# Performance work log

Hardware: AMD Instinct MI355X
Metric: run time of the kernel (lower is better)

## Reference

```python
import jax, jax.numpy as jnp
import numpy as np

N = 100000   # nodes
E = 1000000  # edges (before self-loops)
D_IN = 16
H, C = 2, 64  # heads, hidden per head
EPS = 1e-5    # BatchNorm eps
SLOPE = 0.2   # LeakyReLU negative slope (GATConv default)


def setup_inputs() -> dict:
    key = jax.random.key(0)
    ks = jax.random.split(key, 40)
    rn = lambda k, s, sc=0.1: jax.random.normal(k, s, jnp.float32) * sc
    inp = {}
    inp["x"] = jax.random.normal(ks[0], (N, D_IN), jnp.float32)
    inp["edge_index"] = jax.random.randint(ks[1], (2, E), 0, N)
    i = 2
    for l, din in ((1, D_IN), (2, C), (3, C)):
        inp[f"W{l}"] = rn(ks[i], (din, H * C)); i += 1
        inp[f"as{l}"] = rn(ks[i], (H, C)); i += 1
        inp[f"ad{l}"] = rn(ks[i], (H, C)); i += 1
        inp[f"b{l}"] = jnp.zeros((C,), jnp.float32)
        inp[f"g{l}"] = jnp.ones((C,), jnp.float32)   # BN gamma
        inp[f"be{l}"] = jnp.zeros((C,), jnp.float32) # BN beta
    inp["mW1"] = rn(ks[i], (C + 5, C)); i += 1
    inp["mb1"] = jnp.zeros((C,), jnp.float32)
    inp["mW2"] = rn(ks[i], (C, C)); i += 1
    inp["mb2"] = jnp.zeros((C,), jnp.float32)
    inp["pW"] = rn(ks[i], (C, 1)); i += 1
    inp["pb"] = jnp.zeros((1,), jnp.float32)
    inp["vW"] = rn(ks[i], (C, 1)); i += 1
    inp["vb"] = jnp.zeros((1,), jnp.float32)
    return inp


def gat(x, src, dst, W, att_s, att_d, bias):
    # GATConv, heads=H, concat=False (mean over heads). Messages flow src->dst.
    h = (x @ W).reshape(-1, H, C)               # [N,H,C]
    a_s = jnp.sum(h * att_s, -1)                # [N,H]
    a_d = jnp.sum(h * att_d, -1)                # [N,H]
    e = jax.nn.leaky_relu(a_s[src] + a_d[dst], SLOPE)  # [Etot,H]
    e = e - jax.ops.segment_max(e, dst, num_segments=N)[dst]
    ee = jnp.exp(e)
    alpha = ee / (jax.ops.segment_sum(ee, dst, num_segments=N)[dst] + 1e-16)
    msg = h[src] * alpha[:, :, None]            # [Etot,H,C]
    out = jax.ops.segment_sum(msg, dst, num_segments=N)  # [N,H,C]
    return out.mean(1) + bias                   # [N,C]


def bn(h, g, b):
    m = h.mean(0)
    v = jnp.mean((h - m) ** 2, 0)  # biased variance (torch BN normalization)
    return (h - m) * jax.lax.rsqrt(v + EPS) * g + b


def reference(x, edge_index, W1, as1, ad1, b1, g1, be1,
              W2, as2, ad2, b2, g2, be2, W3, as3, ad3, b3, g3, be3,
              mW1, mb1, mW2, mb2, pW, pb, vW, vb):
    loops = jnp.arange(N)
    src = jnp.concatenate([edge_index[0], loops])  # add_self_loops=True
    dst = jnp.concatenate([edge_index[1], loops])
    ctx = x[:, 9:14]  # context features [N,5]
    h = jax.nn.relu(bn(gat(x, src, dst, W1, as1, ad1, b1), g1, be1))
    h = jax.nn.relu(bn(gat(h, src, dst, W2, as2, ad2, b2), g2, be2))
    h = jax.nn.relu(bn(gat(h, src, dst, W3, as3, ad3, b3), g3, be3))
    # dropout is identity in eval reference
    h = jnp.concatenate([h, ctx], axis=1)          # [N, C+5]
    h = jax.nn.relu(h @ mW1 + mb1) @ mW2 + mb2     # MLP
    logits = (h @ pW + pb).squeeze(-1)             # [N]
    value = (h @ vW + vb).squeeze(-1)              # [N]
    return logits, value
```

## Files before the change

### kernel.cpp

```cpp
#include <hip/hip_runtime.h>
#include <hip/hip_fp16.h>


__device__ __forceinline__ float leaky(float x) { return x > 0.f ? x : 0.2f * x; }

typedef float f32x4 __attribute__((ext_vector_type(4)));

#define BCAP 4096
#define NSL 256

__global__ void bucket_hist(const int* __restrict__ dst, int* __restrict__ bcnt, int E) {
  __shared__ int cnt[512];
  int t = threadIdx.x;
  cnt[t] = 0; cnt[t + 256] = 0;
  __syncthreads();
  for (int e = blockIdx.x * blockDim.x + t; e < E; e += gridDim.x * blockDim.x)
    atomicAdd(&cnt[dst[e] >> 8], 1);
  __syncthreads();
  for (int i = t; i < 512; i += 256)
    if (cnt[i]) atomicAdd(&bcnt[i], cnt[i]);
}

__global__ void bucket_scan(const int* __restrict__ bcnt, int* __restrict__ boff,
                            int* __restrict__ bcur, int nbk) {
  __shared__ int temp[512];
  int t = threadIdx.x;
  int v = (t < nbk) ? bcnt[t] : 0;
  temp[t] = v;
  __syncthreads();
  for (int off = 1; off < 512; off <<= 1) {
    int add = (t >= off) ? temp[t - off] : 0;
    __syncthreads();
    temp[t] += add;
    __syncthreads();
  }
  if (t < nbk) {
    int ex = temp[t] - v;
    boff[t] = ex;
    bcur[t] = ex;
  }
}

__global__ __launch_bounds__(256) void bin_scatter(
    const int* __restrict__ src, const int* __restrict__ dst,
    int* __restrict__ bcur, int2* __restrict__ ebuf, int E) {
  __shared__ int cnt[512];
  __shared__ int base[512];
  int t = threadIdx.x;
  int beg = blockIdx.x * 8192;
  int end = min(E, beg + 8192);
  cnt[t] = 0; cnt[t + 256] = 0;
  __syncthreads();
  for (int e = beg + t; e < end; e += 256)
    atomicAdd(&cnt[dst[e] >> 8], 1);
  __syncthreads();
  for (int i = t; i < 512; i += 256) {
    base[i] = cnt[i] ? atomicAdd(&bcur[i], cnt[i]) : 0;
    cnt[i] = 0;
  }
  __syncthreads();
  for (int e = beg + t; e < end; e += 256) {
    int d = dst[e];
    int bk = d >> 8;
    int off = atomicAdd(&cnt[bk], 1);
    ebuf[base[bk] + off] = make_int2(src[e], d);
  }
}

__global__ __launch_bounds__(256) void bucket_sort(
    const int2* __restrict__ ebuf, const int* __restrict__ boff,
    int2* __restrict__ col2, int* __restrict__ row_ptr, int E, int n, int nbk) {
  __shared__ int2 eds[BCAP];
  __shared__ int dcnt[256];
  __shared__ int dbase[256];
  __shared__ int dexcl[256];
  int b = blockIdx.x, t = threadIdx.x;
  int S = boff[b];
  int Eend = (b + 1 < nbk) ? boff[b + 1] : E;
  int cnt = min(Eend - S, BCAP);
  for (int i = t; i < cnt; i += 256) eds[i] = ebuf[S + i];
  dcnt[t] = 0;
  __syncthreads();
  for (int i = t; i < cnt; i += 256) atomicAdd(&dcnt[eds[i].y & 255], 1);
  __syncthreads();
  int v = dcnt[t];
  dbase[t] = v;
  __syncthreads();
  for (int off = 1; off < 256; off <<= 1) {
    int add = (t >= off) ? dbase[t - off] : 0;
    __syncthreads();
    dbase[t] += add;
    __syncthreads();
  }
  int excl = dbase[t] - v;
  int d = (b << 8) + t;
  if (d < n) row_ptr[d] = S + excl;
  if (b == nbk - 1 && t == 0) row_ptr[n] = E;
  dcnt[t] = 0;
  dexcl[t] = excl;
  __syncthreads();
  for (int i = t; i < cnt; i += 256) {
    int2 e = eds[i];
    int dl = e.y & 255;
    int off = atomicAdd(&dcnt[dl], 1);
    col2[S + dexcl[dl] + off] = e;
  }
}

__global__ __launch_bounds__(256) void bn_stats(const float* __restrict__ h,
                                                float* __restrict__ stats, int n) {
  __shared__ float ssum[64], ssq[64];
  int t = threadIdx.x;
  if (t < 64) { ssum[t] = 0.f; ssq[t] = 0.f; }
  __syncthreads();
  const float4* h4 = (const float4*)h;
  size_t total4 = (size_t)n * 16;
  size_t stride = (size_t)gridDim.x * blockDim.x;
  int cbase = ((int)(((size_t)blockIdx.x * blockDim.x + t) & 15)) * 4;
  float s0 = 0.f, s1 = 0.f, s2 = 0.f, s3 = 0.f;
  float q0 = 0.f, q1 = 0.f, q2 = 0.f, q3 = 0.f;
  for (size_t i = (size_t)blockIdx.x * blockDim.x + t; i < total4; i += stride) {
    float4 v = h4[i];
    s0 += v.x; q0 = fmaf(v.x, v.x, q0);
    s1 += v.y; q1 = fmaf(v.y, v.y, q1);
    s2 += v.z; q2 = fmaf(v.z, v.z, q2);
    s3 += v.w; q3 = fmaf(v.w, v.w, q3);
  }
  atomicAdd(&ssum[cbase + 0], s0); atomicAdd(&ssq[cbase + 0], q0);
  atomicAdd(&ssum[cbase + 1], s1); atomicAdd(&ssq[cbase + 1], q1);
  atomicAdd(&ssum[cbase + 2], s2); atomicAdd(&ssq[cbase + 2], q2);
  atomicAdd(&ssum[cbase + 3], s3); atomicAdd(&ssq[cbase + 3], q3);
  __syncthreads();
  if (t < 64) {
    stats[blockIdx.x * 128 + t] = ssum[t];
    stats[blockIdx.x * 128 + 64 + t] = ssq[t];
  }
}

__global__ void bn_finalize(const float* __restrict__ stats, const float* __restrict__ g,
                            const float* __restrict__ be, float* __restrict__ scsh,
                            float inv_n) {
  __shared__ float red[128];
  int t = threadIdx.x;
  int c = t & 63;
  int off = (t >> 6) * 64;
  float acc = 0.f;
  for (int b = 0; b < NSL; b++) acc += stats[b * 128 + off + c];
  red[t] = acc;
  __syncthreads();
  if (t < 64) {
    float mean = red[t] * inv_n;
    float var = red[64 + t] * inv_n - mean * mean;
    float sc = rsqrtf(var + 1e-5f) * g[t];
    scsh[t] = sc;
    scsh[64 + t] = be[t] - mean * sc;
  }
}

template <int K, bool BN>
__global__ __launch_bounds__(256) void gat_project_tiled(
    const float* __restrict__ act, const float* __restrict__ scsh,
    const float* __restrict__ W,
    const float* __restrict__ att_s, const float* __restrict__ att_d,
    __half2* __restrict__ hb, float* __restrict__ as_,
    float* __restrict__ ad_, int n) {
  constexpr int AST = K + 4;
  __shared__ float aS[64 * AST];
  __shared__ float wS[K * 128];
  __shared__ float attS[256];

  int t = threadIdx.x;
  int node0 = blockIdx.x * 64;
  int rows = min(64, n - node0);

  constexpr int AF4 = 64 * K / 4;
  for (int i = t; i < AF4; i += 256) {
    int r = i / (K / 4), kc = i % (K / 4);
    float4 v = make_float4(0.f, 0.f, 0.f, 0.f);
    if (r < rows) v = *(const float4*)&act[(size_t)(node0 + r) * K + kc * 4];
    if (BN) {
      float4 sc4 = *(const float4*)&scsh[kc * 4];
      float4 sh4 = *(const float4*)&scsh[64 + kc * 4];
      v.x = fmaxf(fmaf(v.x, sc4.x, sh4.x), 0.f);
      v.y = fmaxf(fmaf(v.y, sc4.y, sh4.y), 0.f);
      v.z = fmaxf(fmaf(v.z, sc4.z, sh4.z), 0.f);
      v.w = fmaxf(fmaf(v.w, sc4.w, sh4.w), 0.f);
    }
    *(float4*)&aS[r * AST + kc * 4] = v;
  }
  constexpr int WF4 = K * 32;
  for (int i = t; i < WF4; i += 256)
    *(float4*)&wS[i * 4] = *(const float4*)&W[i * 4];
  attS[t] = (t < 128) ? att_s[t] : att_d[t - 128];
  __syncthreads();

  int tc = t & 15, tr = t >> 4;
  int c0 = tc * 8, r0 = tr * 4;

  float acc[4][8] = {};
  for (int k = 0; k < K; k += 4) {
    float4 av[4];
    float4 wv[4][2];
#pragma unroll
    for (int i = 0; i < 4; i++) av[i] = *(const float4*)&aS[(r0 + i) * AST + k];
#pragma unroll
    for (int kk = 0; kk < 4; kk++) {
      wv[kk][0] = *(const float4*)&wS[(k + kk) * 128 + c0];
      wv[kk][1] = *(const float4*)&wS[(k + kk) * 128 + c0 + 4];
    }
#pragma unroll
    for (int i = 0; i < 4; i++) {
      const float* ai = (const float*)&av[i];
#pragma unroll
      for (int kk = 0; kk < 4; kk++) {
        const float* w0 = (const float*)&wv[kk][0];
        const float* w1 = (const float*)&wv[kk][1];
#pragma unroll
        for (int j = 0; j < 4; j++) {
          acc[i][j] = fmaf(ai[kk], w0[j], acc[i][j]);
          acc[i][4 + j] = fmaf(ai[kk], w1[j], acc[i][4 + j]);
        }
      }
    }
  }

#pragma unroll
  for (int i = 0; i < 4; i++) {
    int r = r0 + i;
    float psv = 0.f, pdv = 0.f;
#pragma unroll
    for (int j = 0; j < 8; j++) {
      psv = fmaf(acc[i][j], attS[c0 + j], psv);
      pdv = fmaf(acc[i][j], attS[128 + c0 + j], pdv);
    }
    psv += __shfl_xor(psv, 1); pdv += __shfl_xor(pdv, 1);
    psv += __shfl_xor(psv, 2); pdv += __shfl_xor(pdv, 2);
    psv += __shfl_xor(psv, 4); pdv += __shfl_xor(pdv, 4);
    if (r < rows) {
      size_t base = (size_t)(node0 + r) * 64 + (c0 >> 1);
      hb[base + 0] = __floats2half2_rn(acc[i][0], acc[i][1]);
      hb[base + 1] = __floats2half2_rn(acc[i][2], acc[i][3]);
      hb[base + 2] = __floats2half2_rn(acc[i][4], acc[i][5]);
      hb[base + 3] = __floats2half2_rn(acc[i][6], acc[i][7]);
      if (tc == 0 || tc == 8) {
        int head = tc >> 3;
        as_[(node0 + r) * 2 + head] = psv;
        ad_[(node0 + r) * 2 + head] = pdv;
      }
    }
  }
}

__device__ __forceinline__ void fma8(float* a, float my, uint4 raw) {
  float2 f;
  f = __half22float2(__builtin_bit_cast(__half2, raw.x)); a[0] = fmaf(my, f.x, a[0]); a[1] = fmaf(my, f.y, a[1]);
  f = __half22float2(__builtin_bit_cast(__half2, raw.y)); a[2] = fmaf(my, f.x, a[2]); a[3] = fmaf(my, f.y, a[3]);
  f = __half22float2(__builtin_bit_cast(__half2, raw.z)); a[4] = fmaf(my, f.x, a[4]); a[5] = fmaf(my, f.y, a[5]);
  f = __half22float2(__builtin_bit_cast(__half2, raw.w)); a[6] = fmaf(my, f.x, a[6]); a[7] = fmaf(my, f.y, a[7]);
}

__global__ __launch_bounds__(256) void gat_aggregate(
    const __half2* __restrict__ hb,
    const float* __restrict__ as_, const float* __restrict__ ad_,
    const int* __restrict__ row_ptr, const int2* __restrict__ col2,
    const float* __restrict__ bias, float* __restrict__ out, int n) {
  int wave = (int)((blockIdx.x * blockDim.x + threadIdx.x) >> 6);
  int lane = threadIdx.x & 63;
  if (wave >= n) return;
  int d = wave;
  int sub = lane >> 4, q = lane & 15;
  bool head1 = (q >= 8);
  int hidx = head1 ? 1 : 0;
  int beg = row_ptr[d], end = row_ptr[d + 1];
  const uint4* hb4 = (const uint4*)hb;

  float2 dv = *(const float2*)&ad_[d * 2];
  float ad_my = head1 ? dv.y : dv.x;

  float a[8] = {};
  float dpart = 0.f;

  if (sub == 0) {
    float asv = as_[d * 2 + hidx];
    float my = __expf(leaky(asv + ad_my));
    uint4 raw = hb4[(size_t)d * 16 + q];
    fma8(a, my, raw);
    dpart = my;
  }

  int k = beg;
  for (; k + 7 < end; k += 8) {
    int kkA = k + sub, kkB = k + 4 + sub;
    int sA = col2[kkA].x;
    int sB = col2[kkB].x;
    float asA = as_[sA * 2 + hidx];
    float asB = as_[sB * 2 + hidx];
    uint4 rawA = hb4[(size_t)sA * 16 + q];
    uint4 rawB = hb4[(size_t)sB * 16 + q];
    float myA = __expf(leaky(asA + ad_my));
    float myB = __expf(leaky(asB + ad_my));
    fma8(a, myA, rawA);
    dpart += myA;
    fma8(a, myB, rawB);
    dpart += myB;
  }
  if (k + 3 < end) {
    int kk = k + sub;
    int s = col2[kk].x;
    float asv = as_[s * 2 + hidx];
    uint4 raw = hb4[(size_t)s * 16 + q];
    float my = __expf(leaky(asv + ad_my));
    fma8(a, my, raw);
    dpart += my;
    k += 4;
  }
  int rem = end - k;
  if (sub < rem) {
    int kk = k + sub;
    int s = col2[kk].x;
    float asv = as_[s * 2 + hidx];
    uint4 raw = hb4[(size_t)s * 16 + q];
    float my = __expf(leaky(asv + ad_my));
    fma8(a, my, raw);
    dpart += my;
  }

#pragma unroll
  for (int i = 0; i < 8; i++) a[i] += __shfl(a[i], lane ^ 16);
  dpart += __shfl(dpart, lane ^ 16);
#pragma unroll
  for (int i = 0; i < 8; i++) a[i] += __shfl(a[i], lane ^ 32);
  float dsum = dpart + __shfl(dpart, lane ^ 32);

  int src = (lane + 8) & 63;
  float b[8];
#pragma unroll
  for (int i = 0; i < 8; i++) b[i] = __shfl(a[i], src);
  float den1 = __shfl(dsum, src);
  if (lane < 8) {
    float r0 = 1.f / (dsum + 1e-16f), r1 = 1.f / (den1 + 1e-16f);
    float4 bl = *(const float4*)&bias[q * 8];
    float4 bh = *(const float4*)&bias[q * 8 + 4];
    f32x4 o0, o1;
    o0.x = 0.5f * (a[0] * r0 + b[0] * r1) + bl.x;
    o0.y = 0.5f * (a[1] * r0 + b[1] * r1) + bl.y;
    o0.z = 0.5f * (a[2] * r0 + b[2] * r1) + bl.z;
    o0.w = 0.5f * (a[3] * r0 + b[3] * r1) + bl.w;
    o1.x = 0.5f * (a[4] * r0 + b[4] * r1) + bh.x;
    o1.y = 0.5f * (a[5] * r0 + b[5] * r1) + bh.y;
    o1.z = 0.5f * (a[6] * r0 + b[6] * r1) + bh.z;
    o1.w = 0.5f * (a[7] * r0 + b[7] * r1) + bh.w;
    f32x4* outp = (f32x4*)&out[(size_t)d * 64 + q * 8];
    __builtin_nontemporal_store(o0, outp);
    __builtin_nontemporal_store(o1, outp + 1);
  }
}

__global__ __launch_bounds__(256) void mlp_head_tiled(
    const float* __restrict__ h3raw, const float* __restrict__ scsh,
    const float* __restrict__ x,
    const float* __restrict__ mW1, const float* __restrict__ mb1,
    const float* __restrict__ mW2, const float* __restrict__ mb2,
    const float* __restrict__ pW, const float* __restrict__ pb,
    const float* __restrict__ vW, const float* __restrict__ vb,
    float* __restrict__ out, int n) {
  __shared__ float lds[13632];
  float* a1  = lds;
  float* ctx = lds + 4352;
  float* a2  = lds + 4864;
  float* w1  = lds + 9216;
  float* w2  = lds;

  int t = threadIdx.x;
  int node0 = blockIdx.x * 64;
  int rows = min(64, n - node0);

#pragma unroll
  for (int i = 0; i < 4; i++) {
    int flat = t + i * 256;
    int r = flat >> 4, kc = flat & 15;
    float4 v = make_float4(0.f, 0.f, 0.f, 0.f);
    if (r < rows) v = *(const float4*)&h3raw[(size_t)(node0 + r) * 64 + kc * 4];
    float4 sc4 = *(const float4*)&scsh[kc * 4];
    float4 sh4 = *(const float4*)&scsh[64 + kc * 4];
    v.x = fmaxf(fmaf(v.x, sc4.x, sh4.x), 0.f);
    v.y = fmaxf(fmaf(v.y, sc4.y, sh4.y), 0.f);
    v.z = fmaxf(fmaf(v.z, sc4.z, sh4.z), 0.f);
    v.w = fmaxf(fmaf(v.w, sc4.w, sh4.w), 0.f);
    *(float4*)&a1[r * 68 + kc * 4] = v;
  }
  for (int i = t; i < 320; i += 256) {
    int r = i / 5, j = i % 5;
    ctx[r * 8 + j] = (r < rows) ? x[(size_t)(node0 + r) * 16 + 9 + j] : 0.f;
  }
#pragma unroll
  for (int i = 0; i < 5; i++) {
    int flat = t + i * 256;
    if (flat < 1104) *(float4*)&w1[flat * 4] = *(const float4*)&mW1[flat * 4];
  }
  __syncthreads();

  int tc = t & 15, tr = t >> 4;
  int c0 = tc * 4, r0 = tr * 4;

  float acc[4][4] = {};
  for (int k = 0; k < 64; k += 4) {
    float4 av[4], wv[4];
#pragma unroll
    for (int i = 0; i < 4; i++) av[i] = *(const float4*)&a1[(r0 + i) * 68 + k];
#pragma unroll
    for (int j = 0; j < 4; j++) wv[j] = *(const float4*)&w1[(k + j) * 64 + c0];
#pragma unroll
    for (int i = 0; i < 4; i++) {
      const float* ai = (const float*)&av[i];
#pragma unroll
      for (int kk = 0; kk < 4; kk++) {
        const float* wr = (const float*)&wv[kk];
        acc[i][0] = fmaf(ai[kk], wr[0], acc[i][0]);
        acc[i][1] = fmaf(ai[kk], wr[1], acc[i][1]);
        acc[i][2] = fmaf(ai[kk], wr[2], acc[i][2]);
        acc[i][3] = fmaf(ai[kk], wr[3], acc[i][3]);
      }
    }
  }
#pragma unroll
  for (int k = 64; k < 69; k++) {
    float4 wv = *(const float4*)&w1[k * 64 + c0];
    const float* wr = (const float*)&wv;
#pragma unroll
    for (int i = 0; i < 4; i++) {
      float a = ctx[(r0 + i) * 8 + (k - 64)];
      acc[i][0] = fmaf(a, wr[0], acc[i][0]);
      acc[i][1] = fmaf(a, wr[1], acc[i][1]);
      acc[i][2] = fmaf(a, wr[2], acc[i][2]);
      acc[i][3] = fmaf(a, wr[3], acc[i][3]);
    }
  }
  float b1v0 = mb1[c0], b1v1 = mb1[c0 + 1], b1v2 = mb1[c0 + 2], b1v3 = mb1[c0 + 3];
#pragma unroll
  for (int i = 0; i < 4; i++) {
    float4 t1;
    t1.x = fmaxf(acc[i][0] + b1v0, 0.f);
    t1.y = fmaxf(acc[i][1] + b1v1, 0.f);
    t1.z = fmaxf(acc[i][2] + b1v2, 0.f);
    t1.w = fmaxf(acc[i][3] + b1v3, 0.f);
    *(float4*)&a2[(r0 + i) * 68 + c0] = t1;
  }
  __syncthreads();

#pragma unroll
  for (int i = 0; i < 4; i++) {
    int flat = t + i * 256;
    *(float4*)&w2[flat * 4] = *(const float4*)&mW2[flat * 4];
  }
  __syncthreads();

  float acc2[4][4] = {};
  for (int k = 0; k < 64; k += 4) {
    float4 av[4], wv[4];
#pragma unroll
    for (int i = 0; i < 4; i++) av[i] = *(const float4*)&a2[(r0 + i) * 68 + k];
#pragma unroll
    for (int j = 0; j < 4; j++) wv[j] = *(const float4*)&w2[(k + j) * 64 + c0];
#pragma unroll
    for (int i = 0; i < 4; i++) {
      const float* ai = (const float*)&av[i];
#pragma unroll
      for (int kk = 0; kk < 4; kk++) {
        const float* wr = (const float*)&wv[kk];
        acc2[i][0] = fmaf(ai[kk], wr[0], acc2[i][0]);
        acc2[i][1] = fmaf(ai[kk], wr[1], acc2[i][1]);
        acc2[i][2] = fmaf(ai[kk], wr[2], acc2[i][2]);
        acc2[i][3] = fmaf(ai[kk], wr[3], acc2[i][3]);
      }
    }
  }

  float b2v[4], pwv[4], vwv[4];
#pragma unroll
  for (int j = 0; j < 4; j++) {
    b2v[j] = mb2[c0 + j];
    pwv[j] = pW[c0 + j];
    vwv[j] = vW[c0 + j];
  }
  float p[4], v[4];
#pragma unroll
  for (int i = 0; i < 4; i++) {
    float ps = 0.f, vs = 0.f;
#pragma unroll
    for (int j = 0; j < 4; j++) {
      float u = acc2[i][j] + b2v[j];
      ps = fmaf(u, pwv[j], ps);
      vs = fmaf(u, vwv[j], vs);
    }
    p[i] = ps; v[i] = vs;
  }
#pragma unroll
  for (int off = 1; off < 16; off <<= 1) {
#pragma unroll
    for (int i = 0; i < 4; i++) {
      p[i] += __shfl_xor(p[i], off);
      v[i] += __shfl_xor(v[i], off);
    }
  }
  if (tc == 0) {
    float pbs = pb[0], vbs = vb[0];
#pragma unroll
    for (int i = 0; i < 4; i++) {
      int r = r0 + i;
      if (r < rows) {
        out[node0 + r] = p[i] + pbs;
        out[n + node0 + r] = v[i] + vbs;
      }
    }
  }
}

extern "C" void kernel_launch(void* const* d_in, const int* in_sizes, int n_in,
                              void* d_out, int out_size, void* d_ws, size_t ws_size,
                              hipStream_t stream) {
  const float* x = (const float*)d_in[0];
  const int* ei = (const int*)d_in[1];
  const float* W[3]  = {(const float*)d_in[2],  (const float*)d_in[8],  (const float*)d_in[14]};
  const float* AS[3] = {(const float*)d_in[3],  (const float*)d_in[9],  (const float*)d_in[15]};
  const float* AD[3] = {(const float*)d_in[4],  (const float*)d_in[10], (const float*)d_in[16]};
  const float* B[3]  = {(const float*)d_in[5],  (const float*)d_in[11], (const float*)d_in[17]};
  const float* G[3]  = {(const float*)d_in[6],  (const float*)d_in[12], (const float*)d_in[18]};
  const float* BE[3] = {(const float*)d_in[7],  (const float*)d_in[13], (const float*)d_in[19]};
  const float* mW1 = (const float*)d_in[20];
  const float* mb1 = (const float*)d_in[21];
  const float* mW2 = (const float*)d_in[22];
  const float* mb2 = (const float*)d_in[23];
  const float* pW  = (const float*)d_in[24];
  const float* pb  = (const float*)d_in[25];
  const float* vW  = (const float*)d_in[26];
  const float* vb  = (const float*)d_in[27];

  const int N = in_sizes[0] / 16;
  const int E = in_sizes[1] / 2;
  const int* srcp = ei;
  const int* dstp = ei + E;

  float* bufB  = (float*)d_ws;
  float* hbuf  = bufB + (size_t)N * 64;
  float* as_   = hbuf + (size_t)N * 64;
  float* ad_   = as_ + (size_t)N * 2;
  float* stats = ad_ + (size_t)N * 2;
  float* scsh  = stats + NSL * 128;
  int* row_ptr = (int*)(scsh + 128);
  int* bcnt    = row_ptr + (N + 1);
  int* boff    = bcnt + 512;
  int* bcur    = boff + 512;
  int2* col2   = (int2*)(bcur + 512);
  int2* ebuf   = col2 + E;
  __half2* hb  = (__half2*)hbuf;

  const int nbk = (N + 255) >> 8;
  const float inv_n = 1.0f / (float)N;

  hipMemsetAsync(bcnt, 0, sizeof(int) * 512, stream);
  bucket_hist<<<256, 256, 0, stream>>>(dstp, bcnt, E);
  bucket_scan<<<1, 512, 0, stream>>>(bcnt, boff, bcur, nbk);
  bin_scatter<<<(E + 8191) / 8192, 256, 0, stream>>>(srcp, dstp, bcur, ebuf, E);
  bucket_sort<<<nbk, 256, 0, stream>>>(ebuf, boff, col2, row_ptr, E, N, nbk);

  const int tiles = (N + 63) / 64;

  for (int l = 0; l < 3; l++) {
    if (l == 0)
      gat_project_tiled<16, false><<<tiles, 256, 0, stream>>>(x, scsh, W[l], AS[l], AD[l],
                                                              hb, as_, ad_, N);
    else
      gat_project_tiled<64, true><<<tiles, 256, 0, stream>>>(bufB, scsh, W[l], AS[l], AD[l],
                                                             hb, as_, ad_, N);
    gat_aggregate<<<(N + 3) / 4, 256, 0, stream>>>(hb, as_, ad_, row_ptr, col2,
                                                   B[l], bufB, N);
    bn_stats<<<NSL, 256, 0, stream>>>(bufB, stats, N);
    bn_finalize<<<1, 128, 0, stream>>>(stats, G[l], BE[l], scsh, inv_n);
  }

  mlp_head_tiled<<<tiles, 256, 0, stream>>>(bufB, scsh, x, mW1, mb1, mW2, mb2,
                                            pW, pb, vW, vb, (float*)d_out, N);
}
```

Measured before the change: 518.1 us.

## Assign one 16-lane group per node in GAT aggregation and store src-only CSR

The aggregation kernel now gives each 16-lane group its own destination node, four nodes per wave, instead of splitting one node's edges across four sub-groups. This removes the cross-subgroup shuffle reductions and the idle lanes on low-degree nodes. The edge loop is unrolled by four to keep several gathers in flight. The sorted CSR column array now holds only source indices (int instead of int2), which halves its footprint and its read traffic. Load imbalance inside a wave is possible when the four nodes have very different degrees.

```diff
diff --git a/kernel.cpp b/kernel.cpp
--- a/kernel.cpp
+++ b/kernel.cpp
@@ -69,7 +69,7 @@
 
 __global__ __launch_bounds__(256) void bucket_sort(
     const int2* __restrict__ ebuf, const int* __restrict__ boff,
-    int2* __restrict__ col2, int* __restrict__ row_ptr, int E, int n, int nbk) {
+    int* __restrict__ col, int* __restrict__ row_ptr, int E, int n, int nbk) {
   __shared__ int2 eds[BCAP];
   __shared__ int dcnt[256];
   __shared__ int dbase[256];
@@ -103,7 +103,7 @@
     int2 e = eds[i];
     int dl = e.y & 255;
     int off = atomicAdd(&dcnt[dl], 1);
-    col2[S + dexcl[dl] + off] = e;
+    col[S + dexcl[dl] + off] = e.x;
   }
 }
 
@@ -262,94 +262,71 @@
 __global__ __launch_bounds__(256) void gat_aggregate(
     const __half2* __restrict__ hb,
     const float* __restrict__ as_, const float* __restrict__ ad_,
-    const int* __restrict__ row_ptr, const int2* __restrict__ col2,
+    const int* __restrict__ row_ptr, const int* __restrict__ col,
     const float* __restrict__ bias, float* __restrict__ out, int n) {
-  int wave = (int)((blockIdx.x * blockDim.x + threadIdx.x) >> 6);
+  int w = (int)((blockIdx.x * blockDim.x + threadIdx.x) >> 6);
   int lane = threadIdx.x & 63;
-  if (wave >= n) return;
-  int d = wave;
-  int sub = lane >> 4, q = lane & 15;
-  bool head1 = (q >= 8);
-  int hidx = head1 ? 1 : 0;
+  int g = lane >> 4, q = lane & 15;
+  int d = w * 4 + g;
+  if (d >= n) return;
+  int hidx = (q >= 8) ? 1 : 0;
   int beg = row_ptr[d], end = row_ptr[d + 1];
   const uint4* hb4 = (const uint4*)hb;
 
-  float2 dv = *(const float2*)&ad_[d * 2];
-  float ad_my = head1 ? dv.y : dv.x;
+  float ad_my = ad_[d * 2 + hidx];
 
   float a[8] = {};
-  float dpart = 0.f;
-
-  if (sub == 0) {
-    float asv = as_[d * 2 + hidx];
-    float my = __expf(leaky(asv + ad_my));
-    uint4 raw = hb4[(size_t)d * 16 + q];
-    fma8(a, my, raw);
-    dpart = my;
-  }
+  float asv = as_[d * 2 + hidx];
+  float my = __expf(leaky(asv + ad_my));
+  uint4 raw = hb4[(size_t)d * 16 + q];
+  fma8(a, my, raw);
+  float dpart = my;
 
   int k = beg;
-  for (; k + 7 < end; k += 8) {
-    int kkA = k + sub, kkB = k + 4 + sub;
-    int sA = col2[kkA].x;
-    int sB = col2[kkB].x;
-    float asA = as_[sA * 2 + hidx];
-    float asB = as_[sB * 2 + hidx];
-    uint4 rawA = hb4[(size_t)sA * 16 + q];
-    uint4 rawB = hb4[(size_t)sB * 16 + q];
-    float myA = __expf(leaky(asA + ad_my));
-    float myB = __expf(leaky(asB + ad_my));
-    fma8(a, myA, rawA);
-    dpart += myA;
-    fma8(a, myB, rawB);
-    dpart += myB;
-  }
-  if (k + 3 < end) {
-    int kk = k + sub;
-    int s = col2[kk].x;
-    float asv = as_[s * 2 + hidx];
-    uint4 raw = hb4[(size_t)s * 16 + q];
-    float my = __expf(leaky(asv + ad_my));
-    fma8(a, my, raw);
-    dpart += my;
-    k += 4;
-  }
-  int rem = end - k;
-  if (sub < rem) {
-    int kk = k + sub;
-    int s = col2[kk].x;
-    float asv = as_[s * 2 + hidx];
-    uint4 raw = hb4[(size_t)s * 16 + q];
-    float my = __expf(leaky(asv + ad_my));
-    fma8(a, my, raw);
-    dpart += my;
-  }
-
-#pragma unroll
-  for (int i = 0; i < 8; i++) a[i] += __shfl(a[i], lane ^ 16);
-  dpart += __shfl(dpart, lane ^ 16);
-#pragma unroll
-  for (int i = 0; i < 8; i++) a[i] += __shfl(a[i], lane ^ 32);
-  float dsum = dpart + __shfl(dpart, lane ^ 32);
-
-  int src = (lane + 8) & 63;
+  for (; k + 3 < end; k += 4) {
+    int s0 = col[k], s1 = col[k + 1], s2 = col[k + 2], s3 = col[k + 3];
+    float e0 = as_[s0 * 2 + hidx];
+    float e1 = as_[s1 * 2 + hidx];
+    float e2 = as_[s2 * 2 + hidx];
+    float e3 = as_[s3 * 2 + hidx];
+    uint4 r0 = hb4[(size_t)s0 * 16 + q];
+    uint4 r1 = hb4[(size_t)s1 * 16 + q];
+    uint4 r2 = hb4[(size_t)s2 * 16 + q];
+    uint4 r3 = hb4[(size_t)s3 * 16 + q];
+    float m0 = __expf(leaky(e0 + ad_my));
+    float m1 = __expf(leaky(e1 + ad_my));
+    float m2 = __expf(leaky(e2 + ad_my));
+    float m3 = __expf(leaky(e3 + ad_my));
+    fma8(a, m0, r0); fma8(a, m1, r1); fma8(a, m2, r2); fma8(a, m3, r3);
+    dpart += m0 + m1 + m2 + m3;
+  }
+  for (; k < end; k++) {
+    int s = col[k];
+    float e = as_[s * 2 + hidx];
+    uint4 r = hb4[(size_t)s * 16 + q];
+    float m = __expf(leaky(e + ad_my));
+    fma8(a, m, r);
+    dpart += m;
+  }
+
   float b[8];
 #pragma unroll
-  for (int i = 0; i < 8; i++) b[i] = __shfl(a[i], src);
-  float den1 = __shfl(dsum, src);
-  if (lane < 8) {
-    float r0 = 1.f / (dsum + 1e-16f), r1 = 1.f / (den1 + 1e-16f);
+  for (int i = 0; i < 8; i++) b[i] = __shfl_xor(a[i], 8);
+  float denO = __shfl_xor(dpart, 8);
+
+  if (q < 8) {
+    float rr0 = 1.f / (dpart + 1e-16f), rr1 = 1.f / (denO + 1e-16f);
     float4 bl = *(const float4*)&bias[q * 8];
     float4 bh = *(const float4*)&bias[q * 8 + 4];
     f32x4 o0, o1;
-    o0.x = 0.5f * (a[0] * r0 + b[0] * r1) + bl.x;
-    o0.y = 0.5f * (a[1] * r0 + b[1] * r1) + bl.y;
-    o0.z = 0.5f * (a[2] * r0 + b[2] * r1) + bl.z;
-    o0.w = 0.5f * (a[3] * r0 + b[3] * r1) + bl.w;
-    o1.x = 0.5f * (a[4] * r0 + b[4] * r1) + bh.x;
-    o1.y = 0.5f * (a[5] * r0 + b[5] * r1) + bh.y;
-    o1.z = 0.5f * (a[6] * r0 + b[6] * r1) + bh.z;
-    o1.w = 0.5f * (a[7] * r0 + b[7] * r1) + bh.w;
+    o0.x = 0.5f * (a[0] * rr0 + b[0] * rr1) + bl.x;
+    o0.y = 0.5f * (a[1] * rr0 + b[1] * rr1) + bl.y;
+    o0.z = 0.5f * (a[2] * rr0 + b[2] * rr1) + bl.z;
+    o0.w = 0.5f * (a[3] * rr0 + b[3] * rr1) + bl.w;
+    o1.x = 0.5f * (a[4] * rr0 + b[4] * rr1) + bh.x;
+    o1.y = 0.5f * (a[5] * rr0 + b[5] * rr1) + bh.y;
+    o1.z = 0.5f * (a[6] * rr0 + b[6] * rr1) + bh.z;
+    o1.w = 0.5f * (a[7] * rr0 + b[7] * rr1) + bh.w;
     f32x4* outp = (f32x4*)&out[(size_t)d * 64 + q * 8];
     __builtin_nontemporal_store(o0, outp);
     __builtin_nontemporal_store(o1, outp + 1);
@@ -551,8 +528,8 @@
   int* bcnt    = row_ptr + (N + 1);
   int* boff    = bcnt + 512;
   int* bcur    = boff + 512;
-  int2* col2   = (int2*)(bcur + 512);
-  int2* ebuf   = col2 + E;
+  int* col     = bcur + 512;
+  int2* ebuf   = (int2*)(col + E);
   __half2* hb  = (__half2*)hbuf;
 
   const int nbk = (N + 255) >> 8;
@@ -562,9 +539,10 @@
   bucket_hist<<<256, 256, 0, stream>>>(dstp, bcnt, E);
   bucket_scan<<<1, 512, 0, stream>>>(bcnt, boff, bcur, nbk);
   bin_scatter<<<(E + 8191) / 8192, 256, 0, stream>>>(srcp, dstp, bcur, ebuf, E);
-  bucket_sort<<<nbk, 256, 0, stream>>>(ebuf, boff, col2, row_ptr, E, N, nbk);
+  bucket_sort<<<nbk, 256, 0, stream>>>(ebuf, boff, col, row_ptr, E, N, nbk);
 
   const int tiles = (N + 63) / 64;
+  const int agg_blocks = (N + 15) / 16;
 
   for (int l = 0; l < 3; l++) {
     if (l == 0)
@@ -573,8 +551,8 @@
     else
       gat_project_tiled<64, true><<<tiles, 256, 0, stream>>>(bufB, scsh, W[l], AS[l], AD[l],
                                                              hb, as_, ad_, N);
-    gat_aggregate<<<(N + 3) / 4, 256, 0, stream>>>(hb, as_, ad_, row_ptr, col2,
-                                                   B[l], bufB, N);
+    gat_aggregate<<<agg_blocks, 256, 0, stream>>>(hb, as_, ad_, row_ptr, col,
+                                                  B[l], bufB, N);
     bn_stats<<<NSL, 256, 0, stream>>>(bufB, stats, N);
     bn_finalize<<<1, 128, 0, stream>>>(stats, G[l], BE[l], scsh, inv_n);
   }
```

After: 488.3 us. 1.06x faster.
